# Optimization experiments

Measured on AMD Instinct MI355X. Metric: run time of the kernel, lower is better.

The kernel has to match this reference:

```python
import jax, jax.numpy as jnp
import numpy as np
import math

B, L, D, H = 8, 1024, 1024, 16  # batch, seq, hidden_dim, num_heads
HD = D // H  # head dim = 64
CLUSTERING = True  # softmax over query axis (dim 1 of [B*H, Lq, Lk])


def setup_inputs() -> dict:
    key = jax.random.key(0)
    ks = jax.random.split(key, 12)
    s = 1.0 / math.sqrt(D)  # torch Linear default init scale-ish
    return {
        "x_q": jax.random.normal(ks[0], (B, L, D), jnp.float32),
        "x_k": jax.random.normal(ks[1], (B, L, D), jnp.float32),
        "x_v": jax.random.normal(ks[2], (B, L, D), jnp.float32),
        "mask": jnp.ones((B, L), dtype=bool),
        "Wq": jax.random.uniform(ks[3], (D, D), jnp.float32, -s, s),
        "bq": jax.random.uniform(ks[4], (D,), jnp.float32, -s, s),
        "Wk": jax.random.uniform(ks[5], (D, D), jnp.float32, -s, s),
        "bk": jax.random.uniform(ks[6], (D,), jnp.float32, -s, s),
        "Wv": jax.random.uniform(ks[7], (D, D), jnp.float32, -s, s),
        "bv": jax.random.uniform(ks[8], (D,), jnp.float32, -s, s),
        "Wo": jax.random.uniform(ks[9], (D, D), jnp.float32, -s, s),
        "bo": jax.random.uniform(ks[10], (D,), jnp.float32, -s, s),
    }


def reference(x_q, x_k, x_v, mask, Wq, bq, Wk, bk, Wv, bv, Wo, bo):
    # Projections (weights stored [in, out])
    Q = x_q @ Wq + bq  # [B, Lq, D]
    K = x_k @ Wk + bk  # [B, Lk, D]
    V = x_v @ Wv + bv  # [B, Lk, D]
    b, lq, _ = Q.shape
    lk = K.shape[1]
    # torch.cat(split(dim_split, 2), dim=0) == reshape to [B, L, H, HD] heads
    Qh = Q.reshape(b, lq, H, HD)
    Kh = K.reshape(b, lk, H, HD)
    Vh = V.reshape(b, lk, H, HD)
    # Scores scaled by sqrt(hidden_dim), NOT sqrt(head_dim) (faithful to source)
    scores = jnp.einsum("bqhd,bkhd->bhqk", Qh, Kh) / math.sqrt(D)
    # NOTE: source computes inf_mask but never applies it -> mask unused.
    if CLUSTERING:
        A = jax.nn.softmax(scores, axis=2)  # softmax over QUERY axis
    else:
        A = jax.nn.softmax(scores, axis=3)  # standard: over key axis
    # dropout ratio 0.0 -> identity
    out = jnp.einsum("bhqk,bkhd->bqhd", A, Vh).reshape(b, lq, D)
    return out @ Wo + bo
```

## Files before the change

kernel.cpp:

```cpp
#include <hip/hip_runtime.h>
#include <hip/hip_bf16.h>

#define B_ 8
#define L_ 1024
#define D_ 1024
#define H_ 16
#define HD_ 64

typedef short short8 __attribute__((ext_vector_type(8)));
typedef float floatx4 __attribute__((ext_vector_type(4)));
typedef unsigned short u16;

__device__ __forceinline__ u16 f2bf(float f) {
  union { float f; unsigned u; } v; v.f = f;
  unsigned r = v.u + 0x7fffu + ((v.u >> 16) & 1u);
  return (u16)(r >> 16);
}
__device__ __forceinline__ unsigned pk2(float a, float b) {
  union { float f; unsigned u; } x, y; x.f = a; y.f = b;
  return __builtin_amdgcn_perm(y.u + 0x8000u, x.u + 0x8000u, 0x07060302u);
}
__device__ __forceinline__ floatx4 mfma16(short8 a, short8 b, floatx4 c) {
  return __builtin_amdgcn_mfma_f32_16x16x32_bf16(a, b, c, 0, 0, 0);
}
__device__ __forceinline__ void gl2lds16(const void* g, void* l) {
  __builtin_amdgcn_global_load_lds(
      (const __attribute__((address_space(1))) void*)g,
      (__attribute__((address_space(3))) void*)l, 16, 0, 0);
}

__global__ __launch_bounds__(256) void cvtx3_k(const float* __restrict__ x0,
    const float* __restrict__ x1, const float* __restrict__ x2,
    u16* __restrict__ y0, u16* __restrict__ y1, u16* __restrict__ y2) {
  const float* x = blockIdx.y == 0 ? x0 : (blockIdx.y == 1 ? x1 : x2);
  u16* y = blockIdx.y == 0 ? y0 : (blockIdx.y == 1 ? y1 : y2);
  size_t i = ((size_t)blockIdx.x * 256 + threadIdx.x) * 8;
  float4 a = *(const float4*)(x + i);
  float4 b = *(const float4*)(x + i + 4);
  uint4 u = make_uint4(pk2(a.x, a.y), pk2(a.z, a.w), pk2(b.x, b.y), pk2(b.z, b.w));
  *(uint4*)(y + i) = u;
}

__global__ __launch_bounds__(256) void cvtw4_k(
    const float* __restrict__ W0, const float* __restrict__ W1,
    const float* __restrict__ W2, const float* __restrict__ W3,
    u16* __restrict__ T0, u16* __restrict__ T1,
    u16* __restrict__ T2, u16* __restrict__ T3) {
  const int z = blockIdx.z;
  const float* W = z == 0 ? W0 : (z == 1 ? W1 : (z == 2 ? W2 : W3));
  u16* Wt = z == 0 ? T0 : (z == 1 ? T1 : (z == 2 ? T2 : T3));
  const int kt = blockIdx.x, nt = blockIdx.y;
  __shared__ __align__(16) u16 t[64 * 72];
  const int tid = threadIdx.x;
  #pragma unroll
  for (int i = 0; i < 4; ++i) {
    int idx = i * 256 + tid;
    int r = idx >> 4, c4 = idx & 15;
    float4 v = *(const float4*)(W + (size_t)(kt * 64 + r) * 1024 + nt * 64 + c4 * 4);
    t[(c4 * 4 + 0) * 72 + r] = f2bf(v.x);
    t[(c4 * 4 + 1) * 72 + r] = f2bf(v.y);
    t[(c4 * 4 + 2) * 72 + r] = f2bf(v.z);
    t[(c4 * 4 + 3) * 72 + r] = f2bf(v.w);
  }
  __syncthreads();
  #pragma unroll
  for (int i = 0; i < 2; ++i) {
    int idx = i * 256 + tid;
    int n = idx >> 3, k8 = idx & 7;
    short8 v = *(const short8*)(&t[n * 72 + k8 * 8]);
    *(short8*)(Wt + (size_t)(nt * 64 + n) * 1024 + kt * 64 + k8 * 8) = v;
  }
}

template<int AMODE, int OUTM>
__global__ __launch_bounds__(256, 2) void gemm2_k(const void* __restrict__ Ap,
    const u16* __restrict__ Bt, const float* __restrict__ bias,
    void* __restrict__ Cp, const float* __restrict__ inv)
{
  const int nt = blockIdx.x, mt = blockIdx.y;
  const int tid = threadIdx.x, lane = tid & 63, w = tid >> 6;
  const int quad = lane >> 4, l16 = lane & 15;
  const int wm = w >> 1, wn = w & 1;
  const int m0 = mt * 128, n0 = nt * 128;

  constexpr int ABYTES = AMODE ? 16384 : 32768;
  constexpr int STG = ABYTES + 16384;
  constexpr int SBYTES = (OUTM == 2 && STG < 34816) ? 34816 : STG;
  __shared__ __align__(16) char smem[SBYTES];
  char* AsB = smem;
  char* BsB = smem + ABYTES;

  const floatx4 fz = {0.f, 0.f, 0.f, 0.f};
  floatx4 acc[4][4];
  #pragma unroll
  for (int i = 0; i < 4; ++i)
    #pragma unroll
    for (int j = 0; j < 4; ++j) acc[i][j] = fz;

  for (int k0 = 0; k0 < 1024; k0 += 64) {
    #pragma unroll
    for (int seg = 0; seg < 4; ++seg) {
      int cI = seg * 256 + w * 64 + lane;
      int r = cI >> 3, sl = cI & 7;
      int kc = sl ^ (r & 7);
      gl2lds16(Bt + (size_t)(n0 + r) * 1024 + k0 + kc * 8, BsB + cI * 16);
    }
    if constexpr (AMODE == 0) {
      const float* A = (const float*)Ap;
      #pragma unroll
      for (int seg = 0; seg < 8; ++seg) {
        int cI = seg * 256 + w * 64 + lane;
        int r = cI >> 4, sl = cI & 15;
        int kc = sl ^ (r & 15);
        gl2lds16(A + (size_t)(m0 + r) * 1024 + k0 + kc * 4, AsB + cI * 16);
      }
    } else {
      const u16* A = (const u16*)Ap;
      #pragma unroll
      for (int seg = 0; seg < 4; ++seg) {
        int cI = seg * 256 + w * 64 + lane;
        int r = cI >> 3, sl = cI & 7;
        int kc = sl ^ (r & 7);
        gl2lds16(A + (size_t)(m0 + r) * 1024 + k0 + kc * 8, AsB + cI * 16);
      }
    }
    __syncthreads();

    #pragma unroll
    for (int ks = 0; ks < 2; ++ks) {
      short8 af[4], bfv[4];
      #pragma unroll
      for (int mf = 0; mf < 4; ++mf) {
        int row = wm * 64 + mf * 16 + l16;
        if constexpr (AMODE == 0) {
          int L0 = ks * 8 + quad * 2;
          float4 x0 = *(const float4*)(AsB + row * 256 + ((L0) ^ l16) * 16);
          float4 x1 = *(const float4*)(AsB + row * 256 + ((L0 + 1) ^ l16) * 16);
          union { uint4 u; short8 s; } uu;
          uu.u = make_uint4(pk2(x0.x, x0.y), pk2(x0.z, x0.w),
                            pk2(x1.x, x1.y), pk2(x1.z, x1.w));
          af[mf] = uu.s;
        } else {
          af[mf] = *(const short8*)(AsB + row * 128 + (((ks * 4 + quad) ^ (l16 & 7)) * 16));
        }
      }
      #pragma unroll
      for (int nf = 0; nf < 4; ++nf) {
        int row = wn * 64 + nf * 16 + l16;
        bfv[nf] = *(const short8*)(BsB + row * 128 + (((ks * 4 + quad) ^ (l16 & 7)) * 16));
      }
      #pragma unroll
      for (int mf = 0; mf < 4; ++mf)
        #pragma unroll
        for (int nf = 0; nf < 4; ++nf)
          acc[mf][nf] = mfma16(af[mf], bfv[nf], acc[mf][nf]);
    }
    __syncthreads();
  }

  float bv[4];
  #pragma unroll
  for (int nf = 0; nf < 4; ++nf) bv[nf] = bias[n0 + wn * 64 + nf * 16 + l16];

  if constexpr (OUTM == 0) {
    float* C = (float*)Cp;
    #pragma unroll
    for (int mf = 0; mf < 4; ++mf)
      #pragma unroll
      for (int nf = 0; nf < 4; ++nf) {
        int n = n0 + wn * 64 + nf * 16 + l16;
        #pragma unroll
        for (int r = 0; r < 4; ++r) {
          int m = m0 + wm * 64 + mf * 16 + quad * 4 + r;
          C[(size_t)m * 1024 + n] = acc[mf][nf][r] + bv[nf];
        }
      }
  } else if constexpr (OUTM == 1) {
    u16* C = (u16*)Cp;
    #pragma unroll
    for (int mf = 0; mf < 4; ++mf)
      #pragma unroll
      for (int nf = 0; nf < 4; ++nf) {
        int n = n0 + wn * 64 + nf * 16 + l16;
        #pragma unroll
        for (int r = 0; r < 4; ++r) {
          int m = m0 + wm * 64 + mf * 16 + quad * 4 + r;
          int bb = m >> 10, l = m & 1023, hh = n >> 6, hd = n & 63;
          C[((size_t)((bb * H_ + hh) * L_) + l) * HD_ + hd] =
              f2bf(acc[mf][nf][r] + bv[nf]);
        }
      }
  } else {
    u16* ct = (u16*)smem;
    const int bb = m0 >> 10;
    const int hrow = bb * 16 + (n0 >> 6) + wn;
    float ivv[4][4];
    #pragma unroll
    for (int mf = 0; mf < 4; ++mf)
      #pragma unroll
      for (int r = 0; r < 4; ++r)
        ivv[mf][r] = inv[(size_t)hrow * 1024 + (m0 & 1023) + wm * 64 + mf * 16 + quad * 4 + r];
    __syncthreads();
    #pragma unroll
    for (int mf = 0; mf < 4; ++mf)
      #pragma unroll
      for (int nf = 0; nf < 4; ++nf)
        #pragma unroll
        for (int r = 0; r < 4; ++r) {
          float val = (acc[mf][nf][r] + bv[nf]) * ivv[mf][r];
          ct[(wn * 64 + nf * 16 + l16) * 136 + wm * 64 + mf * 16 + quad * 4 + r] = f2bf(val);
        }
    __syncthreads();
    u16* Vt = (u16*)Cp;
    #pragma unroll
    for (int i = 0; i < 8; ++i) {
      int cc = i * 256 + tid;
      int n = cc >> 4, l8 = cc & 15;
      int g = l8 >> 2, q2 = l8 & 3;
      int mloc = g * 32 + q2 * 4;
      uint2 lo = *(const uint2*)(&ct[n * 136 + mloc]);
      uint2 hi = *(const uint2*)(&ct[n * 136 + mloc + 16]);
      uint4 uv = make_uint4(lo.x, lo.y, hi.x, hi.y);
      *(uint4*)(Vt + ((size_t)bb * 1024 + n0 + n) * 1024 + (m0 & 1023) + l8 * 8) = uv;
    }
  }
}

__global__ __launch_bounds__(256, 2) void colsum2_k(const u16* __restrict__ Q,
    const u16* __restrict__ K, float* __restrict__ inv)
{
  const int ktb = blockIdx.x, h = blockIdx.y, b = blockIdx.z;
  const int tid = threadIdx.x, lane = tid & 63, w = tid >> 6;
  const int quad = lane >> 4, l16 = lane & 15;
  const size_t hb = (size_t)(b * H_ + h) * L_ * HD_;
  const u16* Qh = Q + hb;
  const u16* Kh = K + hb;
  const int kbase = ktb * 256 + w * 64;
  const floatx4 fz = {0.f, 0.f, 0.f, 0.f};
  const float cexp = 0.04508422f;

  __shared__ __align__(16) u16 qsm[16384];

  short8 kf[4][2];
  #pragma unroll
  for (int nf = 0; nf < 4; ++nf)
    #pragma unroll
    for (int ks = 0; ks < 2; ++ks)
      kf[nf][ks] = *(const short8*)(Kh + (size_t)(kbase + nf * 16 + l16) * 64 + ks * 32 + quad * 8);

  float cs[4] = {0.f, 0.f, 0.f, 0.f};
  for (int qc = 0; qc < 4; ++qc) {
    #pragma unroll
    for (int seg = 0; seg < 8; ++seg) {
      int cI = seg * 256 + w * 64 + lane;
      int row = cI >> 3, sl = cI & 7;
      gl2lds16(Qh + (size_t)(qc * 256 + row) * 64 + ((sl ^ (row & 7)) * 8), (char*)qsm + cI * 16);
    }
    __syncthreads();
    #pragma unroll
    for (int mf = 0; mf < 16; ++mf) {
      short8 qf0 = *(const short8*)(&qsm[(mf * 16 + l16) * 64 + ((quad ^ (l16 & 7)) * 8)]);
      short8 qf1 = *(const short8*)(&qsm[(mf * 16 + l16) * 64 + (((4 + quad) ^ (l16 & 7)) * 8)]);
      floatx4 sacc[4];
      #pragma unroll
      for (int nf = 0; nf < 4; ++nf) {
        floatx4 s = mfma16(qf0, kf[nf][0], fz);
        sacc[nf] = mfma16(qf1, kf[nf][1], s);
      }
      #pragma unroll
      for (int nf = 0; nf < 4; ++nf)
        #pragma unroll
        for (int r = 0; r < 4; ++r)
          cs[nf] += __builtin_amdgcn_exp2f(sacc[nf][r] * cexp);
    }
    __syncthreads();
  }
  #pragma unroll
  for (int nf = 0; nf < 4; ++nf) {
    cs[nf] += __shfl_xor(cs[nf], 16);
    cs[nf] += __shfl_xor(cs[nf], 32);
  }
  if (quad == 0) {
    #pragma unroll
    for (int nf = 0; nf < 4; ++nf)
      inv[(size_t)(b * H_ + h) * L_ + kbase + nf * 16 + l16] = 1.0f / cs[nf];
  }
}

__global__ __launch_bounds__(256, 2) void attn3_k(const u16* __restrict__ Q,
    const u16* __restrict__ K, const u16* __restrict__ Vt, u16* __restrict__ O)
{
  const int qb = blockIdx.x, h = blockIdx.y, b = blockIdx.z;
  const int tid = threadIdx.x, lane = tid & 63, w = tid >> 6;
  const int quad = lane >> 4, l16 = lane & 15;
  const size_t hb = (size_t)(b * H_ + h) * L_ * HD_;
  const u16* Qh = Q + hb;
  const u16* Kh = K + hb;
  const u16* Vh = Vt + ((size_t)b * D_ + h * HD_) * L_;
  const int q0 = qb * 256 + w * 64;
  const floatx4 fz = {0.f, 0.f, 0.f, 0.f};
  const float cexp = 0.04508422f;

  __shared__ __align__(16) u16 smem[18432];
  u16* ksb = smem;
  u16* vsb = smem + 8192;

  short8 qf[4][2];
  #pragma unroll
  for (int qs = 0; qs < 4; ++qs)
    #pragma unroll
    for (int ks = 0; ks < 2; ++ks)
      qf[qs][ks] = *(const short8*)(Qh + (size_t)(q0 + qs * 16 + l16) * 64 + ks * 32 + quad * 8);

  floatx4 oT[4][4];
  #pragma unroll
  for (int i = 0; i < 4; ++i)
    #pragma unroll
    for (int j = 0; j < 4; ++j) oT[i][j] = fz;

  for (int kc = 0; kc < 8; ++kc) {
    const int kk = kc * 128;
    #pragma unroll
    for (int seg = 0; seg < 4; ++seg) {
      int cI = seg * 256 + w * 64 + lane;
      int row = cI >> 3, sl = cI & 7;
      gl2lds16(Kh + (size_t)(kk + row) * 64 + ((sl ^ (row & 7)) * 8), (char*)ksb + cI * 16);
    }
    #pragma unroll
    for (int seg = 0; seg < 4; ++seg) {
      int cI = seg * 256 + w * 64 + lane;
      int row = cI >> 4, sl = cI & 15;
      gl2lds16(Vh + (size_t)row * L_ + kk + ((sl ^ (row & 15)) * 8), (char*)vsb + cI * 16);
    }
    __syncthreads();

    #pragma unroll
    for (int p = 0; p < 4; ++p) {
      short8 ka0[2], ka1[2];
      #pragma unroll
      for (int ks = 0; ks < 2; ++ks) {
        ka0[ks] = *(const short8*)((char*)ksb + (p * 32 + l16) * 128 + (((ks * 4 + quad) ^ (l16 & 7)) * 16));
        ka1[ks] = *(const short8*)((char*)ksb + (p * 32 + 16 + l16) * 128 + (((ks * 4 + quad) ^ (l16 & 7)) * 16));
      }
      short8 pt[4];
      #pragma unroll
      for (int qs = 0; qs < 4; ++qs) {
        floatx4 s0 = mfma16(ka0[0], qf[qs][0], fz);
        s0 = mfma16(ka0[1], qf[qs][1], s0);
        floatx4 s1 = mfma16(ka1[0], qf[qs][0], fz);
        s1 = mfma16(ka1[1], qf[qs][1], s1);
        float e0 = __builtin_amdgcn_exp2f(s0[0] * cexp);
        float e1 = __builtin_amdgcn_exp2f(s0[1] * cexp);
        float e2 = __builtin_amdgcn_exp2f(s0[2] * cexp);
        float e3 = __builtin_amdgcn_exp2f(s0[3] * cexp);
        float f0 = __builtin_amdgcn_exp2f(s1[0] * cexp);
        float f1 = __builtin_amdgcn_exp2f(s1[1] * cexp);
        float f2 = __builtin_amdgcn_exp2f(s1[2] * cexp);
        float f3 = __builtin_amdgcn_exp2f(s1[3] * cexp);
        union { uint4 u; short8 s; } pu;
        pu.u = make_uint4(pk2(e0, e1), pk2(e2, e3), pk2(f0, f1), pk2(f2, f3));
        pt[qs] = pu.s;
      }
      #pragma unroll
      for (int ds = 0; ds < 4; ++ds) {
        short8 va = *(const short8*)((char*)vsb + (ds * 16 + l16) * 256 + (((p * 4 + quad) ^ l16) * 16));
        #pragma unroll
        for (int qs = 0; qs < 4; ++qs)
          oT[ds][qs] = mfma16(va, pt[qs], oT[ds][qs]);
      }
    }
    __syncthreads();
  }

  u16* ot = smem + w * 4608;
  #pragma unroll
  for (int ds = 0; ds < 4; ++ds)
    #pragma unroll
    for (int qs = 0; qs < 4; ++qs)
      #pragma unroll
      for (int r = 0; r < 4; ++r)
        ot[(qs * 16 + l16) * 72 + ds * 16 + quad * 4 + r] = f2bf(oT[ds][qs][r]);
  __syncthreads();
  #pragma unroll
  for (int i = 0; i < 8; ++i) {
    int cc = i * 64 + lane;
    int ql = cc >> 3, d8 = cc & 7;
    short8 v = *(const short8*)(&ot[ql * 72 + d8 * 8]);
    *(short8*)(O + ((size_t)b * L_ + q0 + ql) * D_ + h * HD_ + d8 * 8) = v;
  }
}

extern "C" void kernel_launch(void* const* d_in, const int* in_sizes, int n_in,
                              void* d_out, int out_size, void* d_ws, size_t ws_size,
                              hipStream_t stream) {
  const float* xq = (const float*)d_in[0];
  const float* xk = (const float*)d_in[1];
  const float* xv = (const float*)d_in[2];
  const float* Wq = (const float*)d_in[4];
  const float* bq = (const float*)d_in[5];
  const float* Wk = (const float*)d_in[6];
  const float* bk = (const float*)d_in[7];
  const float* Wv = (const float*)d_in[8];
  const float* bv = (const float*)d_in[9];
  const float* Wo = (const float*)d_in[10];
  const float* bo = (const float*)d_in[11];

  char* ws = (char*)d_ws;
  const size_t MB = 1u << 20;
  dim3 blk(256);
  dim3 gg(8, 64);

  if (ws_size >= 90 * MB) {
    u16* xqb = (u16*)(ws);
    u16* xkb = (u16*)(ws + 16 * MB);
    u16* xvb = (u16*)(ws + 32 * MB);
    u16* WTq = (u16*)(ws + 48 * MB);
    u16* WTk = (u16*)(ws + 50 * MB);
    u16* WTv = (u16*)(ws + 52 * MB);
    u16* WTo = (u16*)(ws + 54 * MB);
    float* invb = (float*)(ws + 56 * MB);
    u16* Qb = (u16*)(ws + 57 * MB);
    u16* Kb = (u16*)(ws + 73 * MB);
    u16* Vtb = (u16*)(ws);
    u16* Ob = (u16*)(ws + 16 * MB);

    cvtx3_k<<<dim3(4096, 3), blk, 0, stream>>>(xq, xk, xv, xqb, xkb, xvb);
    cvtw4_k<<<dim3(16, 16, 4), blk, 0, stream>>>(Wq, Wk, Wv, Wo, WTq, WTk, WTv, WTo);
    gemm2_k<1, 1><<<gg, blk, 0, stream>>>(xqb, WTq, bq, Qb, nullptr);
    gemm2_k<1, 1><<<gg, blk, 0, stream>>>(xkb, WTk, bk, Kb, nullptr);
    colsum2_k<<<dim3(4, 16, 8), blk, 0, stream>>>(Qb, Kb, invb);
    gemm2_k<1, 2><<<gg, blk, 0, stream>>>(xvb, WTv, bv, Vtb, invb);
    attn3_k<<<dim3(4, 16, 8), blk, 0, stream>>>(Qb, Kb, Vtb, Ob);
    gemm2_k<1, 0><<<gg, blk, 0, stream>>>(Ob, WTo, bo, (float*)d_out, nullptr);
  } else {
    const size_t MB16 = 16u << 20;
    u16* Xbf  = (u16*)(ws);
    u16* Vtb  = (u16*)(ws);
    u16* Qb   = (u16*)(ws + MB16);
    u16* WT2  = (u16*)(ws + MB16);
    u16* Kb   = (u16*)(ws + 2 * MB16);
    u16* WT   = (u16*)(ws + 3 * MB16);
    float* invb = (float*)(ws + 3 * MB16 + (2u << 20));
    u16* Ob   = (u16*)(ws + 3 * MB16);

    cvtx3_k<<<dim3(4096, 1), blk, 0, stream>>>(xq, xq, xq, Xbf, Xbf, Xbf);
    cvtw4_k<<<dim3(16, 16, 1), blk, 0, stream>>>(Wq, Wq, Wq, Wq, WT, WT, WT, WT);
    gemm2_k<1, 1><<<gg, blk, 0, stream>>>(Xbf, WT, bq, Qb, nullptr);
    cvtx3_k<<<dim3(4096, 1), blk, 0, stream>>>(xk, xk, xk, Xbf, Xbf, Xbf);
    cvtw4_k<<<dim3(16, 16, 1), blk, 0, stream>>>(Wk, Wk, Wk, Wk, WT, WT, WT, WT);
    gemm2_k<1, 1><<<gg, blk, 0, stream>>>(Xbf, WT, bk, Kb, nullptr);
    colsum2_k<<<dim3(4, 16, 8), blk, 0, stream>>>(Qb, Kb, invb);
    cvtw4_k<<<dim3(16, 16, 1), blk, 0, stream>>>(Wv, Wv, Wv, Wv, WT, WT, WT, WT);
    gemm2_k<0, 2><<<gg, blk, 0, stream>>>(xv, WT, bv, Vtb, invb);
    attn3_k<<<dim3(4, 16, 8), blk, 0, stream>>>(Qb, Kb, Vtb, Ob);
    cvtw4_k<<<dim3(16, 16, 1), blk, 0, stream>>>(Wo, Wo, Wo, Wo, WT2, WT2, WT2, WT2);
    gemm2_k<1, 0><<<gg, blk, 0, stream>>>(Ob, WT2, bo, (float*)d_out, nullptr);
  }
}
```

Before: 335.9 us.

## Fold softmax scale into K projection, double-buffer attention LDS, reorder grids

The K projection epilogue now multiplies by the exp2 softmax scale, so colsum and attention drop the per-element multiply before exp2. The attention kernel double-buffers its K/V LDS tiles, issuing the next chunk's loads before computing on the current one. Grid dimensions for the GEMMs, colsum and attention are swapped so consecutive blocks walk M or heads first, which changes L2 reuse. The larger LDS footprint (64KB) may cut occupancy, and rounding K to bf16 after scaling slightly changes numerics.

```diff
diff --git a/kernel.cpp b/kernel.cpp
--- a/kernel.cpp
+++ b/kernel.cpp
@@ -28,6 +28,8 @@
       (const __attribute__((address_space(1))) void*)g,
       (__attribute__((address_space(3))) void*)l, 16, 0, 0);
 }
+
+#define KSCALE 0.04508422f
 
 __global__ __launch_bounds__(256) void cvtx3_k(const float* __restrict__ x0,
     const float* __restrict__ x1, const float* __restrict__ x2,
@@ -75,9 +77,9 @@
 template<int AMODE, int OUTM>
 __global__ __launch_bounds__(256, 2) void gemm2_k(const void* __restrict__ Ap,
     const u16* __restrict__ Bt, const float* __restrict__ bias,
-    void* __restrict__ Cp, const float* __restrict__ inv)
+    void* __restrict__ Cp, const float* __restrict__ inv, float scale)
 {
-  const int nt = blockIdx.x, mt = blockIdx.y;
+  const int mt = blockIdx.x, nt = blockIdx.y;
   const int tid = threadIdx.x, lane = tid & 63, w = tid >> 6;
   const int quad = lane >> 4, l16 = lane & 15;
   const int wm = w >> 1, wn = w & 1;
@@ -187,7 +189,7 @@
           int m = m0 + wm * 64 + mf * 16 + quad * 4 + r;
           int bb = m >> 10, l = m & 1023, hh = n >> 6, hd = n & 63;
           C[((size_t)((bb * H_ + hh) * L_) + l) * HD_ + hd] =
-              f2bf(acc[mf][nf][r] + bv[nf]);
+              f2bf((acc[mf][nf][r] + bv[nf]) * scale);
         }
       }
   } else {
@@ -229,15 +231,14 @@
 __global__ __launch_bounds__(256, 2) void colsum2_k(const u16* __restrict__ Q,
     const u16* __restrict__ K, float* __restrict__ inv)
 {
-  const int ktb = blockIdx.x, h = blockIdx.y, b = blockIdx.z;
+  const int hh = blockIdx.x, ktb = blockIdx.y;
   const int tid = threadIdx.x, lane = tid & 63, w = tid >> 6;
   const int quad = lane >> 4, l16 = lane & 15;
-  const size_t hb = (size_t)(b * H_ + h) * L_ * HD_;
+  const size_t hb = (size_t)hh * L_ * HD_;
   const u16* Qh = Q + hb;
   const u16* Kh = K + hb;
   const int kbase = ktb * 256 + w * 64;
   const floatx4 fz = {0.f, 0.f, 0.f, 0.f};
-  const float cexp = 0.04508422f;
 
   __shared__ __align__(16) u16 qsm[16384];
 
@@ -271,7 +272,7 @@
       for (int nf = 0; nf < 4; ++nf)
         #pragma unroll
         for (int r = 0; r < 4; ++r)
-          cs[nf] += __builtin_amdgcn_exp2f(sacc[nf][r] * cexp);
+          cs[nf] += __builtin_amdgcn_exp2f(sacc[nf][r]);
     }
     __syncthreads();
   }
@@ -283,27 +284,25 @@
   if (quad == 0) {
     #pragma unroll
     for (int nf = 0; nf < 4; ++nf)
-      inv[(size_t)(b * H_ + h) * L_ + kbase + nf * 16 + l16] = 1.0f / cs[nf];
+      inv[(size_t)hh * L_ + kbase + nf * 16 + l16] = 1.0f / cs[nf];
   }
 }
 
 __global__ __launch_bounds__(256, 2) void attn3_k(const u16* __restrict__ Q,
     const u16* __restrict__ K, const u16* __restrict__ Vt, u16* __restrict__ O)
 {
-  const int qb = blockIdx.x, h = blockIdx.y, b = blockIdx.z;
+  const int hh = blockIdx.x, qb = blockIdx.y;
+  const int b = hh >> 4, h = hh & 15;
   const int tid = threadIdx.x, lane = tid & 63, w = tid >> 6;
   const int quad = lane >> 4, l16 = lane & 15;
-  const size_t hb = (size_t)(b * H_ + h) * L_ * HD_;
+  const size_t hb = (size_t)hh * L_ * HD_;
   const u16* Qh = Q + hb;
   const u16* Kh = K + hb;
   const u16* Vh = Vt + ((size_t)b * D_ + h * HD_) * L_;
   const int q0 = qb * 256 + w * 64;
   const floatx4 fz = {0.f, 0.f, 0.f, 0.f};
-  const float cexp = 0.04508422f;
-
-  __shared__ __align__(16) u16 smem[18432];
-  u16* ksb = smem;
-  u16* vsb = smem + 8192;
+
+  __shared__ __align__(16) u16 smem[32768];
 
   short8 qf[4][2];
   #pragma unroll
@@ -318,29 +317,39 @@
     #pragma unroll
     for (int j = 0; j < 4; ++j) oT[i][j] = fz;
 
-  for (int kc = 0; kc < 8; ++kc) {
+  auto stage = [&](int kc, int buf) {
     const int kk = kc * 128;
+    char* kdst = (char*)smem + buf * 32768;
+    char* vdst = kdst + 16384;
     #pragma unroll
     for (int seg = 0; seg < 4; ++seg) {
       int cI = seg * 256 + w * 64 + lane;
       int row = cI >> 3, sl = cI & 7;
-      gl2lds16(Kh + (size_t)(kk + row) * 64 + ((sl ^ (row & 7)) * 8), (char*)ksb + cI * 16);
+      gl2lds16(Kh + (size_t)(kk + row) * 64 + ((sl ^ (row & 7)) * 8), kdst + cI * 16);
     }
     #pragma unroll
     for (int seg = 0; seg < 4; ++seg) {
       int cI = seg * 256 + w * 64 + lane;
       int row = cI >> 4, sl = cI & 15;
-      gl2lds16(Vh + (size_t)row * L_ + kk + ((sl ^ (row & 15)) * 8), (char*)vsb + cI * 16);
-    }
-    __syncthreads();
+      gl2lds16(Vh + (size_t)row * L_ + kk + ((sl ^ (row & 15)) * 8), vdst + cI * 16);
+    }
+  };
+
+  stage(0, 0);
+  __syncthreads();
+  int buf = 0;
+  for (int kc = 0; kc < 8; ++kc) {
+    if (kc < 7) stage(kc + 1, buf ^ 1);
+    char* ksb = (char*)smem + buf * 32768;
+    char* vsb = ksb + 16384;
 
     #pragma unroll
     for (int p = 0; p < 4; ++p) {
       short8 ka0[2], ka1[2];
       #pragma unroll
       for (int ks = 0; ks < 2; ++ks) {
-        ka0[ks] = *(const short8*)((char*)ksb + (p * 32 + l16) * 128 + (((ks * 4 + quad) ^ (l16 & 7)) * 16));
-        ka1[ks] = *(const short8*)((char*)ksb + (p * 32 + 16 + l16) * 128 + (((ks * 4 + quad) ^ (l16 & 7)) * 16));
+        ka0[ks] = *(const short8*)(ksb + (p * 32 + l16) * 128 + (((ks * 4 + quad) ^ (l16 & 7)) * 16));
+        ka1[ks] = *(const short8*)(ksb + (p * 32 + 16 + l16) * 128 + (((ks * 4 + quad) ^ (l16 & 7)) * 16));
       }
       short8 pt[4];
       #pragma unroll
@@ -349,27 +358,28 @@
         s0 = mfma16(ka0[1], qf[qs][1], s0);
         floatx4 s1 = mfma16(ka1[0], qf[qs][0], fz);
         s1 = mfma16(ka1[1], qf[qs][1], s1);
-        float e0 = __builtin_amdgcn_exp2f(s0[0] * cexp);
-        float e1 = __builtin_amdgcn_exp2f(s0[1] * cexp);
-        float e2 = __builtin_amdgcn_exp2f(s0[2] * cexp);
-        float e3 = __builtin_amdgcn_exp2f(s0[3] * cexp);
-        float f0 = __builtin_amdgcn_exp2f(s1[0] * cexp);
-        float f1 = __builtin_amdgcn_exp2f(s1[1] * cexp);
-        float f2 = __builtin_amdgcn_exp2f(s1[2] * cexp);
-        float f3 = __builtin_amdgcn_exp2f(s1[3] * cexp);
+        float e0 = __builtin_amdgcn_exp2f(s0[0]);
+        float e1 = __builtin_amdgcn_exp2f(s0[1]);
+        float e2 = __builtin_amdgcn_exp2f(s0[2]);
+        float e3 = __builtin_amdgcn_exp2f(s0[3]);
+        float f0 = __builtin_amdgcn_exp2f(s1[0]);
+        float f1 = __builtin_amdgcn_exp2f(s1[1]);
+        float f2 = __builtin_amdgcn_exp2f(s1[2]);
+        float f3 = __builtin_amdgcn_exp2f(s1[3]);
         union { uint4 u; short8 s; } pu;
         pu.u = make_uint4(pk2(e0, e1), pk2(e2, e3), pk2(f0, f1), pk2(f2, f3));
         pt[qs] = pu.s;
       }
       #pragma unroll
       for (int ds = 0; ds < 4; ++ds) {
-        short8 va = *(const short8*)((char*)vsb + (ds * 16 + l16) * 256 + (((p * 4 + quad) ^ l16) * 16));
+        short8 va = *(const short8*)(vsb + (ds * 16 + l16) * 256 + (((p * 4 + quad) ^ l16) * 16));
         #pragma unroll
         for (int qs = 0; qs < 4; ++qs)
           oT[ds][qs] = mfma16(va, pt[qs], oT[ds][qs]);
       }
     }
     __syncthreads();
+    buf ^= 1;
   }
 
   u16* ot = smem + w * 4608;
@@ -408,7 +418,7 @@
   char* ws = (char*)d_ws;
   const size_t MB = 1u << 20;
   dim3 blk(256);
-  dim3 gg(8, 64);
+  dim3 gg(64, 8);
 
   if (ws_size >= 90 * MB) {
     u16* xqb = (u16*)(ws);
@@ -426,12 +436,12 @@
 
     cvtx3_k<<<dim3(4096, 3), blk, 0, stream>>>(xq, xk, xv, xqb, xkb, xvb);
     cvtw4_k<<<dim3(16, 16, 4), blk, 0, stream>>>(Wq, Wk, Wv, Wo, WTq, WTk, WTv, WTo);
-    gemm2_k<1, 1><<<gg, blk, 0, stream>>>(xqb, WTq, bq, Qb, nullptr);
-    gemm2_k<1, 1><<<gg, blk, 0, stream>>>(xkb, WTk, bk, Kb, nullptr);
-    colsum2_k<<<dim3(4, 16, 8), blk, 0, stream>>>(Qb, Kb, invb);
-    gemm2_k<1, 2><<<gg, blk, 0, stream>>>(xvb, WTv, bv, Vtb, invb);
-    attn3_k<<<dim3(4, 16, 8), blk, 0, stream>>>(Qb, Kb, Vtb, Ob);
-    gemm2_k<1, 0><<<gg, blk, 0, stream>>>(Ob, WTo, bo, (float*)d_out, nullptr);
+    gemm2_k<1, 1><<<gg, blk, 0, stream>>>(xqb, WTq, bq, Qb, nullptr, 1.0f);
+    gemm2_k<1, 1><<<gg, blk, 0, stream>>>(xkb, WTk, bk, Kb, nullptr, KSCALE);
+    colsum2_k<<<dim3(128, 4), blk, 0, stream>>>(Qb, Kb, invb);
+    gemm2_k<1, 2><<<gg, blk, 0, stream>>>(xvb, WTv, bv, Vtb, invb, 1.0f);
+    attn3_k<<<dim3(128, 4), blk, 0, stream>>>(Qb, Kb, Vtb, Ob);
+    gemm2_k<1, 0><<<gg, blk, 0, stream>>>(Ob, WTo, bo, (float*)d_out, nullptr, 1.0f);
   } else {
     const size_t MB16 = 16u << 20;
     u16* Xbf  = (u16*)(ws);
@@ -445,15 +455,15 @@
 
     cvtx3_k<<<dim3(4096, 1), blk, 0, stream>>>(xq, xq, xq, Xbf, Xbf, Xbf);
     cvtw4_k<<<dim3(16, 16, 1), blk, 0, stream>>>(Wq, Wq, Wq, Wq, WT, WT, WT, WT);
-    gemm2_k<1, 1><<<gg, blk, 0, stream>>>(Xbf, WT, bq, Qb, nullptr);
+    gemm2_k<1, 1><<<gg, blk, 0, stream>>>(Xbf, WT, bq, Qb, nullptr, 1.0f);
     cvtx3_k<<<dim3(4096, 1), blk, 0, stream>>>(xk, xk, xk, Xbf, Xbf, Xbf);
     cvtw4_k<<<dim3(16, 16, 1), blk, 0, stream>>>(Wk, Wk, Wk, Wk, WT, WT, WT, WT);
-    gemm2_k<1, 1><<<gg, blk, 0, stream>>>(Xbf, WT, bk, Kb, nullptr);
-    colsum2_k<<<dim3(4, 16, 8), blk, 0, stream>>>(Qb, Kb, invb);
+    gemm2_k<1, 1><<<gg, blk, 0, stream>>>(Xbf, WT, bk, Kb, nullptr, KSCALE);
+    colsum2_k<<<dim3(128, 4), blk, 0, stream>>>(Qb, Kb, invb);
     cvtw4_k<<<dim3(16, 16, 1), blk, 0, stream>>>(Wv, Wv, Wv, Wv, WT, WT, WT, WT);
-    gemm2_k<0, 2><<<gg, blk, 0, stream>>>(xv, WT, bv, Vtb, invb);
-    attn3_k<<<dim3(4, 16, 8), blk, 0, stream>>>(Qb, Kb, Vtb, Ob);
+    gemm2_k<0, 2><<<gg, blk, 0, stream>>>(xv, WT, bv, Vtb, invb, 1.0f);
+    attn3_k<<<dim3(128, 4), blk, 0, stream>>>(Qb, Kb, Vtb, Ob);
     cvtw4_k<<<dim3(16, 16, 1), blk, 0, stream>>>(Wo, Wo, Wo, Wo, WT2, WT2, WT2, WT2);
-    gemm2_k<1, 0><<<gg, blk, 0, stream>>>(Ob, WT2, bo, (float*)d_out, nullptr);
-  }
-}
+    gemm2_k<1, 0><<<gg, blk, 0, stream>>>(Ob, WT2, bo, (float*)d_out, nullptr, 1.0f);
+  }
+}
```

New measurement: 314.9 us. 1.07x faster.
